# Optimization experiments

Measured on AMD Instinct MI355X. Metric: run time of the kernel, lower is better.

The kernel has to match this reference:

```python
import jax, jax.numpy as jnp
import numpy as np
from jax import lax

T, N, CIN, CMID, IMG, LABELS = 8, 32, 3, 64, 64, 10
W4 = IMG // 4  # 16 after two 2x2 maxpools
FC1_IN = CMID * W4 * W4                 # 16384
FC1_OUT = (CMID * W4 // 2) * W4 // 2    # 4096 (matches Python int-div precedence)
V_TH = 1.0
ALPHA = 4.0  # spikingjelly surrogate.Sigmoid default alpha

@jax.custom_vjp
def spike(x):
    # Heaviside(v - v_th); surrogate sigmoid gradient in bwd
    return (x >= 0.0).astype(x.dtype)

def _spike_fwd(x):
    return (x >= 0.0).astype(x.dtype), x

def _spike_bwd(x, g):
    s = jax.nn.sigmoid(ALPHA * x)
    return (g * ALPHA * s * (1.0 - s),)

spike.defvjp(_spike_fwd, _spike_bwd)

def if_node(x_seq):
    # IFNode, hard reset to v_reset=0, v starts at 0, multi-step over leading T axis
    def step(v, x):
        v = v + x                 # charge
        s = spike(v - V_TH)       # fire
        return v * (1.0 - s), s   # hard reset (reset path keeps grad: detach_reset=False)
    _, s_seq = lax.scan(step, jnp.zeros_like(x_seq[0]), x_seq)
    return s_seq

def conv2d(x, w):
    # kernel 3x3, stride 1, padding 1, no bias
    return lax.conv_general_dilated(x, w, (1, 1), ((1, 1), (1, 1)),
                                    dimension_numbers=('NCHW', 'OIHW', 'NCHW'))

def maxpool2(x):
    return lax.reduce_window(x, -jnp.inf, lax.max, (1, 1, 2, 2), (1, 1, 2, 2), 'VALID')

def seq_apply(f, x_seq):
    # stateless layer applied over merged [T*N, ...] (spikingjelly step_mode='m')
    t, n = x_seq.shape[:2]
    y = f(x_seq.reshape((t * n,) + x_seq.shape[2:]))
    return y.reshape((t, n) + y.shape[1:])


def setup_inputs() -> dict:
    key = jax.random.key(0)
    k = jax.random.split(key, 5)
    x_seq = jax.random.uniform(k[0], (T, N, CIN, IMG, IMG), dtype=jnp.float32)
    w1 = jax.random.normal(k[1], (CMID, CIN, 3, 3), dtype=jnp.float32) * (1.0 / np.sqrt(CIN * 9))
    w2 = jax.random.normal(k[2], (CMID, CMID, 3, 3), dtype=jnp.float32) * (1.0 / np.sqrt(CMID * 9))
    fc1 = jax.random.normal(k[3], (FC1_OUT, FC1_IN), dtype=jnp.float32) * (1.0 / np.sqrt(FC1_IN))
    fc2 = jax.random.normal(k[4], (LABELS, FC1_OUT), dtype=jnp.float32) * (1.0 / np.sqrt(FC1_OUT))
    return {"x_seq": x_seq, "w1": w1, "w2": w2, "fc1": fc1, "fc2": fc2}


def reference(x_seq, w1, w2, fc1, fc2):
    h = seq_apply(lambda x: conv2d(x, w1), x_seq)   # [T,N,64,64,64]
    h = if_node(h)
    h = seq_apply(maxpool2, h)                      # [T,N,64,32,32]
    h = seq_apply(lambda x: conv2d(x, w2), h)
    h = if_node(h)
    h = seq_apply(maxpool2, h)                      # [T,N,64,16,16]
    h = h.reshape(T, N, -1)                         # [T,N,16384]
    h = if_node(jnp.einsum('tni,oi->tno', h, fc1))  # [T,N,4096]
    h = if_node(jnp.einsum('tni,oi->tno', h, fc2))  # [T,N,10]
    return h.mean(axis=0)                           # firing rate over time: [N,10]
```

## Files before the change

### kernel.cpp

```cpp
#include <hip/hip_runtime.h>
#include <hip/hip_bf16.h>


#define T_STEPS 8
#define NB      32
#define CMID    64

typedef __bf16 bf16x2 __attribute__((ext_vector_type(2)));
typedef __bf16 bf16x4 __attribute__((ext_vector_type(4)));
typedef __bf16 bf16x8 __attribute__((ext_vector_type(8)));
typedef short  s16x8  __attribute__((ext_vector_type(8)));
typedef float  f32x4  __attribute__((ext_vector_type(4)));

struct Split3 { float h, m, l; };
__device__ __forceinline__ Split3 split3(float x) {
    Split3 s;
    __bf16 h = (__bf16)x;
    float r1 = x - (float)h;
    __bf16 m = (__bf16)r1;
    float r2 = r1 - (float)m;
    __bf16 l = (__bf16)r2;
    s.h = (float)h; s.m = (float)m; s.l = (float)l;
    return s;
}

__device__ __forceinline__ void split3v8(float4 a, float4 b,
                                         s16x8& fh, s16x8& fm, s16x8& fl) {
    float x[8] = {a.x, a.y, a.z, a.w, b.x, b.y, b.z, b.w};
    s16x8 h, m, l;
#pragma unroll
    for (int j = 0; j < 8; j++) {
        __bf16 ch = (__bf16)x[j];
        float r1 = x[j] - (float)ch;
        __bf16 cm = (__bf16)r1;
        float r2 = r1 - (float)cm;
        __bf16 cl = (__bf16)r2;
        h[j] = __builtin_bit_cast(short, ch);
        m[j] = __builtin_bit_cast(short, cm);
        l[j] = __builtin_bit_cast(short, cl);
    }
    fh = h; fm = m; fl = l;
}

__device__ __forceinline__ void load_lds16(const void* g, void* l) {
    __builtin_amdgcn_global_load_lds(
        (const __attribute__((address_space(1))) void*)g,
        (__attribute__((address_space(3))) void*)l, 16, 0, 0);
}

__global__ void k_w2s(const float* __restrict__ w2, __bf16* __restrict__ w2s) {
    int idx = blockIdx.x * 256 + threadIdx.x;
    int j    = idx & 7;
    int lane = (idx >> 3) & 63;
    int oh   = (idx >> 9) & 1;
    int kh   = (idx >> 10) & 1;
    int g    = idx >> 11;
    int tap  = g % 9;
    int ch   = g / 9;
    int co = ch * 32 + oh * 16 + (lane & 15);
    int ci = kh * 32 + (lane >> 4) * 8 + j;
    float w = w2[co * 576 + ci * 9 + tap];
    Split3 s = split3(w);
    __bf16* o = w2s + (((size_t)(g * 2 + kh) * 2 + oh) * 3) * 512 + lane * 8 + j;
    o[0]    = (__bf16)s.h;
    o[512]  = (__bf16)s.m;
    o[1024] = (__bf16)s.l;
}

__global__ __launch_bounds__(256) void k_conv1_if_pool(
        const float* __restrict__ x, const float* __restrict__ w1,
        __bf16* __restrict__ spk1p) {
    int b   = blockIdx.x;
    int n   = b >> 5;
    int cog = (b >> 2) & 7;
    int pht = b & 3;
    int tid = threadIdx.x;
    int pw  = tid & 31;
    int ph  = pht * 8 + (tid >> 5);
    int ih0 = 2 * ph - 1, iw0 = 2 * pw - 1;

    float v[8][4];
#pragma unroll
    for (int a = 0; a < 8; a++)
#pragma unroll
        for (int p = 0; p < 4; p++) v[a][p] = 0.f;

    for (int t = 0; t < T_STEPS; t++) {
        const float* xb = x + (size_t)(t * NB + n) * 3 * 4096;
        float patch[3][4][4];
#pragma unroll
        for (int ci = 0; ci < 3; ci++)
#pragma unroll
            for (int dy = 0; dy < 4; dy++) {
                int ih = ih0 + dy;
                bool rok = ((unsigned)ih < 64u);
#pragma unroll
                for (int dx = 0; dx < 4; dx++) {
                    int iw = iw0 + dx;
                    patch[ci][dy][dx] = (rok && ((unsigned)iw < 64u))
                                            ? xb[ci * 4096 + ih * 64 + iw] : 0.f;
                }
            }
        bf16x8 sv;
#pragma unroll
        for (int c8 = 0; c8 < 8; c8++) {
            int co = cog * 8 + c8;
            const float* wc = w1 + co * 27;
            float a0 = 0.f, a1 = 0.f, a2 = 0.f, a3 = 0.f;
#pragma unroll
            for (int ci = 0; ci < 3; ci++)
#pragma unroll
                for (int ky = 0; ky < 3; ky++)
#pragma unroll
                    for (int kx = 0; kx < 3; kx++) {
                        float w = wc[ci * 9 + ky * 3 + kx];
                        a0 += w * patch[ci][ky][kx];
                        a1 += w * patch[ci][ky][kx + 1];
                        a2 += w * patch[ci][ky + 1][kx];
                        a3 += w * patch[ci][ky + 1][kx + 1];
                    }
            float s0, s1, s2, s3;
            v[c8][0] += a0; s0 = (v[c8][0] >= 1.f) ? 1.f : 0.f; if (s0 > 0.f) v[c8][0] = 0.f;
            v[c8][1] += a1; s1 = (v[c8][1] >= 1.f) ? 1.f : 0.f; if (s1 > 0.f) v[c8][1] = 0.f;
            v[c8][2] += a2; s2 = (v[c8][2] >= 1.f) ? 1.f : 0.f; if (s2 > 0.f) v[c8][2] = 0.f;
            v[c8][3] += a3; s3 = (v[c8][3] >= 1.f) ? 1.f : 0.f; if (s3 > 0.f) v[c8][3] = 0.f;
            sv[c8] = (__bf16)fmaxf(fmaxf(s0, s1), fmaxf(s2, s3));
        }
        *(bf16x8*)(spk1p + ((size_t)(t * NB + n) * 1024 + ph * 32 + pw) * 64
                         + cog * 8) = sv;
    }
}

__global__ __launch_bounds__(512, 2) void k_conv2_if_pool(
        const short* __restrict__ spk1p,
        const short* __restrict__ w2s,
        __bf16* __restrict__ spk2) {
    int b     = blockIdx.x;
    int ch    = b & 1;
    int s2    = (b >> 1) & 3;
    int n     = b >> 3;
    int tid   = threadIdx.x;
    int lane  = tid & 63;
    int wv    = tid >> 6;
    int mh    = wv >> 1, oh = wv & 1;
    int lm    = lane & 15, kq = lane >> 4;

    __shared__ short Bs[55296];
    __shared__ short As[10 * 34 * 64];

    {
        const uint4* src = (const uint4*)(w2s + (size_t)ch * 55296);
        uint4* dst = (uint4*)Bs;
        for (int i = tid; i < 6912; i += 512) dst[i] = src[i];
        uint4* za = (uint4*)As;
        for (int i = tid; i < 2720; i += 512) za[i] = (uint4){0, 0, 0, 0};
    }
    __syncthreads();
    const short* Bsw = Bs + oh * 1536;

    int wl  = lane >> 3;
    int sph = lane & 7;

    f32x4 v[4];
#pragma unroll
    for (int i = 0; i < 4; i++) v[i] = (f32x4){0.f, 0.f, 0.f, 0.f};

    int co = ch * 32 + oh * 16 + lm;
    int pH = s2 * 4 + mh;

#pragma unroll 1
    for (int t = 0; t < T_STEPS; t++) {
        const short* img = spk1p + (size_t)(t * NB + n) * 65536;

        if (t > 0) __syncthreads();
#pragma unroll
        for (int q = 0; q < 5; q++) {
            int u = q * 8 + wv;
            int r = u >> 2;
            int quarter = u & 3;
            int hh = s2 * 8 - 1 + r;
            if ((unsigned)hh < 32u) {
                int widx = quarter * 8 + 1 + wl;
                int slog = sph ^ (widx & 7);
                const short* src = img + (size_t)(hh * 32 + widx - 1) * 64
                                       + slog * 8;
                short* dst = As + (r * 34 + quarter * 8 + 1) * 64;
                load_lds16(src, dst);
            }
        }
        __syncthreads();

        f32x4 acc[4];
#pragma unroll
        for (int i = 0; i < 4; i++) acc[i] = (f32x4){0.f, 0.f, 0.f, 0.f};

#pragma unroll 1
        for (int dy = 0; dy < 3; dy++) {
#pragma unroll 1
            for (int dx = 0; dx < 3; dx++) {
                const short* bp = Bsw + (dy * 3 + dx) * 6144 + lane * 8;
                s16x8 bf[2][3];
#pragma unroll
                for (int kh = 0; kh < 2; kh++)
#pragma unroll
                    for (int sp = 0; sp < 3; sp++)
                        bf[kh][sp] = *(const s16x8*)(bp + kh * 3072 + sp * 512);
#pragma unroll
                for (int i = 0; i < 4; i++) {
                    int r    = 2 * mh + (i >> 1) + dy;
                    int widx = (i & 1) * 16 + lm + dx;
                    const short* ap = As + (r * 34 + widx) * 64;
                    s16x8 a0 = *(const s16x8*)(ap + ((kq    ) ^ (widx & 7)) * 8);
                    s16x8 a1 = *(const s16x8*)(ap + ((kq + 4) ^ (widx & 7)) * 8);
#pragma unroll
                    for (int sp = 0; sp < 3; sp++) {
                        acc[i] = __builtin_amdgcn_mfma_f32_16x16x32_bf16(
                            a0, bf[0][sp], acc[i], 0, 0, 0);
                        acc[i] = __builtin_amdgcn_mfma_f32_16x16x32_bf16(
                            a1, bf[1][sp], acc[i], 0, 0, 0);
                    }
                }
            }
        }
        float s[4][4];
#pragma unroll
        for (int i = 0; i < 4; i++)
#pragma unroll
            for (int r = 0; r < 4; r++) {
                float vv = v[i][r] + acc[i][r];
                float sp = (vv >= 1.f) ? 1.f : 0.f;
                s[i][r] = sp;
                v[i][r] = (sp > 0.f) ? 0.f : vv;
            }
        __bf16* op = spk2 + ((size_t)(t * NB + n) * 64 + co) * 256 + pH * 16
                   + kq * 2;
#pragma unroll
        for (int i2 = 0; i2 < 2; i2++) {
            float p0 = fmaxf(fmaxf(s[i2][0], s[i2][1]),
                             fmaxf(s[i2 + 2][0], s[i2 + 2][1]));
            float p1 = fmaxf(fmaxf(s[i2][2], s[i2][3]),
                             fmaxf(s[i2 + 2][2], s[i2 + 2][3]));
            bf16x2 pv = {(__bf16)p0, (__bf16)p1};
            *(bf16x2*)(op + i2 * 8) = pv;
        }
    }
}

__global__ __launch_bounds__(512, 4) void k_fc1_mfma(
        const short* __restrict__ A,
        const float* __restrict__ W,
        float* __restrict__ part) {
    int b  = blockIdx.x;
    int nt = b & 63;
    int ks = b >> 6;
    int o0 = nt * 64;
    int kbase = ks * 2048;

    int tid  = threadIdx.x;
    int lane = tid & 63;
    int wv   = tid >> 6;
    int mq   = wv >> 1;
    int oh   = wv & 1;
    int lm   = lane & 15;
    int kq   = lane >> 4;

    __shared__ short Asm[3][8192];
    __shared__ float Wsm[3][2048];

    int wrow = tid >> 3;
    int wu   = (tid & 7) ^ (wrow & 7);
    const float* gW = W + (size_t)(o0 + wrow) * 16384 + kbase + wu * 4;
    const short* gA[2];
#pragma unroll
    for (int q = 0; q < 2; q++) {
        int p = q * 512 + tid;
        int r = p >> 2;
        int c = (p & 3) ^ ((r >> 1) & 3);
        gA[q] = A + (size_t)r * 16384 + kbase + c * 8;
    }

    int aoff[4];
#pragma unroll
    for (int i = 0; i < 4; i++) {
        int r = mq * 64 + i * 16 + lm;
        aoff[i] = (r * 4 + (kq ^ ((r >> 1) & 3))) * 8;
    }
    int woff[2][2];
#pragma unroll
    for (int oi = 0; oi < 2; oi++) {
        int row = (2 * oh + oi) * 16 + lm;
#pragma unroll
        for (int h = 0; h < 2; h++) {
            int u = kq * 2 + h;
            woff[oi][h] = (row * 8 + (u ^ (row & 7))) * 4;
        }
    }

    f32x4 acc[4][2];
#pragma unroll
    for (int i = 0; i < 4; i++)
#pragma unroll
        for (int oi = 0; oi < 2; oi++) acc[i][oi] = (f32x4){0.f, 0.f, 0.f, 0.f};

    load_lds16(gW,         &Wsm[0][wv * 256]);
    load_lds16(gA[0],      &Asm[0][wv * 512]);
    load_lds16(gA[1],      &Asm[0][4096 + wv * 512]);
    load_lds16(gW + 32,    &Wsm[1][wv * 256]);
    load_lds16(gA[0] + 32, &Asm[1][wv * 512]);
    load_lds16(gA[1] + 32, &Asm[1][4096 + wv * 512]);
    asm volatile("s_waitcnt vmcnt(3)" ::: "memory");
    __builtin_amdgcn_s_barrier();
    __builtin_amdgcn_sched_barrier(0);

#pragma unroll 1
    for (int it = 0; it < 64; ++it) {
        int cur = it % 3;
        if (it < 62) {
            int nb = (it + 2) % 3;
            load_lds16(gW + (it + 2) * 32,    &Wsm[nb][wv * 256]);
            load_lds16(gA[0] + (it + 2) * 32, &Asm[nb][wv * 512]);
            load_lds16(gA[1] + (it + 2) * 32, &Asm[nb][4096 + wv * 512]);
        }

        const short* as = Asm[cur];
        const float* ws = Wsm[cur];

        s16x8 av[4];
#pragma unroll
        for (int i = 0; i < 4; i++)
            av[i] = *(const s16x8*)(as + aoff[i]);

        float4 wraw[2][2];
#pragma unroll
        for (int oi = 0; oi < 2; oi++)
#pragma unroll
            for (int h = 0; h < 2; h++)
                wraw[oi][h] = *(const float4*)(ws + woff[oi][h]);

        s16x8 bfr[3][2];
#pragma unroll
        for (int oi = 0; oi < 2; oi++)
            split3v8(wraw[oi][0], wraw[oi][1],
                     bfr[0][oi], bfr[1][oi], bfr[2][oi]);

#pragma unroll
        for (int i = 0; i < 4; i++)
#pragma unroll
            for (int oi = 0; oi < 2; oi++) {
                acc[i][oi] = __builtin_amdgcn_mfma_f32_16x16x32_bf16(
                    av[i], bfr[0][oi], acc[i][oi], 0, 0, 0);
                acc[i][oi] = __builtin_amdgcn_mfma_f32_16x16x32_bf16(
                    av[i], bfr[1][oi], acc[i][oi], 0, 0, 0);
                acc[i][oi] = __builtin_amdgcn_mfma_f32_16x16x32_bf16(
                    av[i], bfr[2][oi], acc[i][oi], 0, 0, 0);
            }

        if (it < 62) {
            asm volatile("s_waitcnt vmcnt(3)" ::: "memory");
            __builtin_amdgcn_s_barrier();
            __builtin_amdgcn_sched_barrier(0);
        } else if (it == 62) {
            asm volatile("s_waitcnt vmcnt(0)" ::: "memory");
            __builtin_amdgcn_s_barrier();
            __builtin_amdgcn_sched_barrier(0);
        }
    }

    int col = lane & 15;
    int rq  = (lane >> 4) * 4;
#pragma unroll
    for (int i = 0; i < 4; i++)
#pragma unroll
        for (int oi = 0; oi < 2; oi++)
#pragma unroll
            for (int r = 0; r < 4; r++) {
                int m = mq * 64 + i * 16 + rq + r;
                int o = o0 + (2 * oh + oi) * 16 + col;
                part[((size_t)ks * 256 + m) * 4096 + o] = acc[i][oi][r];
            }
}

__global__ void k_fc1_if(const float* __restrict__ part,
                         float* __restrict__ spk3) {
    int idx = blockIdx.x * 256 + threadIdx.x;
    int o = idx & 4095;
    int n = idx >> 12;
    float v = 0.f;
    for (int t = 0; t < T_STEPS; t++) {
        int m = t * NB + n;
        float s = 0.f;
#pragma unroll
        for (int ks = 0; ks < 8; ks++)
            s += part[((size_t)ks * 256 + m) * 4096 + o];
        v += s;
        float sp = (v >= 1.f) ? 1.f : 0.f;
        if (sp > 0.f) v = 0.f;
        spk3[(size_t)m * 4096 + o] = sp;
    }
}

__global__ __launch_bounds__(256) void k_fc2_if_mean(
        const float* __restrict__ spk3, const float* __restrict__ fc2,
        float* __restrict__ out) {
    int b = blockIdx.x;
    int n = b / 10, o = b % 10;
    const float* wr = fc2 + o * 4096;
    __shared__ float red[256];
    int tid = threadIdx.x;
    float v = 0.f, cnt = 0.f;
    for (int t = 0; t < T_STEPS; t++) {
        const float* row = spk3 + (size_t)(t * NB + n) * 4096;
        float p = 0.f;
        for (int i = tid; i < 4096; i += 256) p += row[i] * wr[i];
        red[tid] = p;
        __syncthreads();
        for (int s = 128; s > 0; s >>= 1) {
            if (tid < s) red[tid] += red[tid + s];
            __syncthreads();
        }
        if (tid == 0) {
            v += red[0];
            float sp = (v >= 1.f) ? 1.f : 0.f;
            cnt += sp;
            if (sp > 0.f) v = 0.f;
        }
        __syncthreads();
    }
    if (tid == 0) out[n * 10 + o] = cnt * 0.125f;
}

extern "C" void kernel_launch(void* const* d_in, const int* in_sizes, int n_in,
                              void* d_out, int out_size, void* d_ws, size_t ws_size,
                              hipStream_t stream) {
    const float* x   = (const float*)d_in[0];
    const float* w1  = (const float*)d_in[1];
    const float* w2  = (const float*)d_in[2];
    const float* fc1 = (const float*)d_in[3];
    const float* fc2 = (const float*)d_in[4];
    float* out = (float*)d_out;

    float* ws = (float*)d_ws;
    const size_t off_w2s   = 0;
    const size_t off_spk1p = 57344;
    const size_t off_spk2  = off_spk1p + 8388608;
    const size_t off_part  = off_spk2 + 2097152;
    const size_t off_spk3  = off_part + 8388608;
    __bf16* w2s   = (__bf16*)(ws + off_w2s);
    __bf16* spk1p = (__bf16*)(ws + off_spk1p);
    __bf16* spk2  = (__bf16*)(ws + off_spk2);
    float*  part  = ws + off_part;
    float*  spk3  = ws + off_spk3;

    k_w2s<<<144, 256, 0, stream>>>(w2, w2s);
    k_conv1_if_pool<<<1024, 256, 0, stream>>>(x, w1, spk1p);
    k_conv2_if_pool<<<256, 512, 0, stream>>>((const short*)spk1p,
                                             (const short*)w2s, spk2);
    k_fc1_mfma<<<512, 512, 0, stream>>>((const short*)spk2, fc1, part);
    k_fc1_if<<<512, 256, 0, stream>>>(part, spk3);
    k_fc2_if_mean<<<320, 256, 0, stream>>>(spk3, fc2, out);
}
```

Before: 643.6 us.

## Load fc1 A operand directly into registers, double-buffered, bypassing LDS

The fc1 MFMA kernel no longer stages the bf16 activation tile through shared memory. Each wave now reads its A fragments straight from global memory into registers, double-buffered across iterations, while W keeps the 3-stage LDS pipeline with adjusted vmcnt waits. MFMA sections are also wrapped in s_setprio to favour the math waves. This frees LDS (which may raise occupancy) and removes LDS reads for A, at the cost of uncoalesced 16-byte global loads and more registers.

New measurement: 680.4 us. 1.06x slower.

```diff
diff --git a/kernel.cpp b/kernel.cpp
--- a/kernel.cpp
+++ b/kernel.cpp
@@ -264,27 +264,14 @@
     int lm   = lane & 15;
     int kq   = lane >> 4;
 
-    __shared__ short Asm[3][8192];
     __shared__ float Wsm[3][2048];
 
     int wrow = tid >> 3;
     int wu   = (tid & 7) ^ (wrow & 7);
     const float* gW = W + (size_t)(o0 + wrow) * 16384 + kbase + wu * 4;
-    const short* gA[2];
-#pragma unroll
-    for (int q = 0; q < 2; q++) {
-        int p = q * 512 + tid;
-        int r = p >> 2;
-        int c = (p & 3) ^ ((r >> 1) & 3);
-        gA[q] = A + (size_t)r * 16384 + kbase + c * 8;
-    }
-
-    int aoff[4];
-#pragma unroll
-    for (int i = 0; i < 4; i++) {
-        int r = mq * 64 + i * 16 + lm;
-        aoff[i] = (r * 4 + (kq ^ ((r >> 1) & 3))) * 8;
-    }
+
+    const short* gAf = A + (size_t)(mq * 64 + lm) * 16384 + kbase + kq * 8;
+
     int woff[2][2];
 #pragma unroll
     for (int oi = 0; oi < 2; oi++) {
@@ -302,68 +289,68 @@
 #pragma unroll
         for (int oi = 0; oi < 2; oi++) acc[i][oi] = (f32x4){0.f, 0.f, 0.f, 0.f};
 
-    load_lds16(gW,         &Wsm[0][wv * 256]);
-    load_lds16(gA[0],      &Asm[0][wv * 512]);
-    load_lds16(gA[1],      &Asm[0][4096 + wv * 512]);
-    load_lds16(gW + 32,    &Wsm[1][wv * 256]);
-    load_lds16(gA[0] + 32, &Asm[1][wv * 512]);
-    load_lds16(gA[1] + 32, &Asm[1][4096 + wv * 512]);
-    asm volatile("s_waitcnt vmcnt(3)" ::: "memory");
+    s16x8 avA[4], avB[4];
+
+    load_lds16(gW,      &Wsm[0][wv * 256]);
+    load_lds16(gW + 32, &Wsm[1][wv * 256]);
+    __builtin_amdgcn_sched_barrier(0);
+#pragma unroll
+    for (int i = 0; i < 4; i++)
+        avA[i] = *(const s16x8*)(gAf + (size_t)i * 16 * 16384);
+    asm volatile("s_waitcnt vmcnt(5)" ::: "memory");
     __builtin_amdgcn_s_barrier();
     __builtin_amdgcn_sched_barrier(0);
 
-#pragma unroll 1
-    for (int it = 0; it < 64; ++it) {
-        int cur = it % 3;
-        if (it < 62) {
-            int nb = (it + 2) % 3;
-            load_lds16(gW + (it + 2) * 32,    &Wsm[nb][wv * 256]);
-            load_lds16(gA[0] + (it + 2) * 32, &Asm[nb][wv * 512]);
-            load_lds16(gA[1] + (it + 2) * 32, &Asm[nb][4096 + wv * 512]);
-        }
-
-        const short* as = Asm[cur];
-        const float* ws = Wsm[cur];
-
-        s16x8 av[4];
-#pragma unroll
-        for (int i = 0; i < 4; i++)
-            av[i] = *(const s16x8*)(as + aoff[i]);
-
+    auto body = [&](int it, s16x8* avc, s16x8* avn) {
+        if (it < 62)
+            load_lds16(gW + (it + 2) * 32, &Wsm[(it + 2) % 3][wv * 256]);
+        __builtin_amdgcn_sched_barrier(0);
+        if (it < 63) {
+            const short* ga = gAf + (it + 1) * 32;
+#pragma unroll
+            for (int i = 0; i < 4; i++)
+                avn[i] = *(const s16x8*)(ga + (size_t)i * 16 * 16384);
+        }
+        const float* ws = Wsm[it % 3];
         float4 wraw[2][2];
 #pragma unroll
         for (int oi = 0; oi < 2; oi++)
 #pragma unroll
             for (int h = 0; h < 2; h++)
                 wraw[oi][h] = *(const float4*)(ws + woff[oi][h]);
-
         s16x8 bfr[3][2];
 #pragma unroll
         for (int oi = 0; oi < 2; oi++)
             split3v8(wraw[oi][0], wraw[oi][1],
                      bfr[0][oi], bfr[1][oi], bfr[2][oi]);
-
+        __builtin_amdgcn_s_setprio(1);
 #pragma unroll
         for (int i = 0; i < 4; i++)
 #pragma unroll
             for (int oi = 0; oi < 2; oi++) {
                 acc[i][oi] = __builtin_amdgcn_mfma_f32_16x16x32_bf16(
-                    av[i], bfr[0][oi], acc[i][oi], 0, 0, 0);
+                    avc[i], bfr[0][oi], acc[i][oi], 0, 0, 0);
                 acc[i][oi] = __builtin_amdgcn_mfma_f32_16x16x32_bf16(
-                    av[i], bfr[1][oi], acc[i][oi], 0, 0, 0);
+                    avc[i], bfr[1][oi], acc[i][oi], 0, 0, 0);
                 acc[i][oi] = __builtin_amdgcn_mfma_f32_16x16x32_bf16(
-                    av[i], bfr[2][oi], acc[i][oi], 0, 0, 0);
-            }
-
+                    avc[i], bfr[2][oi], acc[i][oi], 0, 0, 0);
+            }
+        __builtin_amdgcn_s_setprio(0);
         if (it < 62) {
-            asm volatile("s_waitcnt vmcnt(3)" ::: "memory");
+            asm volatile("s_waitcnt vmcnt(5)" ::: "memory");
             __builtin_amdgcn_s_barrier();
             __builtin_amdgcn_sched_barrier(0);
         } else if (it == 62) {
-            asm volatile("s_waitcnt vmcnt(0)" ::: "memory");
+            asm volatile("s_waitcnt vmcnt(4)" ::: "memory");
             __builtin_amdgcn_s_barrier();
             __builtin_amdgcn_sched_barrier(0);
         }
+    };
+
+#pragma unroll 1
+    for (int j = 0; j < 32; ++j) {
+        body(2 * j,     avA, avB);
+        body(2 * j + 1, avB, avA);
     }
 
     int col = lane & 15;
```
